# Performance work log

Measured on AMD Instinct MI355X. Metric: run time of the kernel, lower is better.

The kernel has to match this reference:

```python
import jax, jax.numpy as jnp
import numpy as np

S, T, D, H = 16384, 16, 128, 3   # statements, AST nodes per statement, feat dim, heads
N = S * T
EPS = 1e-5


def setup_inputs() -> dict:
    key = jax.random.key(0)
    k = jax.random.split(key, 12)
    idx = np.arange(N)
    child = idx[idx % T != 0]                      # chain edges child->parent within each AST
    src = jnp.asarray(np.concatenate([child, idx]), dtype=jnp.int32)       # + self loops
    dst = jnp.asarray(np.concatenate([child - 1, idx]), dtype=jnp.int32)
    sD = 1.0 / np.sqrt(D)
    s3D = 1.0 / np.sqrt(3.0 * D)
    return dict(
        x=jax.random.normal(k[0], (N, D), jnp.float32),
        W0=jax.random.normal(k[1], (D, H * D), jnp.float32) * sD,
        a_src0=jax.random.normal(k[2], (H, D), jnp.float32) * sD,
        a_dst0=jax.random.normal(k[3], (H, D), jnp.float32) * sD,
        b0=jnp.zeros((H * D,), jnp.float32),
        g0=jnp.ones((H * D,), jnp.float32),
        be0=jnp.zeros((H * D,), jnp.float32),
        W1=jax.random.normal(k[4], (H * D, D), jnp.float32) * s3D,
        a_src1=jax.random.normal(k[5], (1, D), jnp.float32) * sD,
        a_dst1=jax.random.normal(k[6], (1, D), jnp.float32) * sD,
        b1=jnp.zeros((D,), jnp.float32),
        g1=jnp.ones((D,), jnp.float32),
        be1=jnp.zeros((D,), jnp.float32),
        p=jax.random.normal(k[7], (D,), jnp.float32),
        mW1=jax.random.normal(k[8], (D, 32), jnp.float32) * sD,
        mb1=jnp.zeros((32,), jnp.float32),
        mW2=jax.random.normal(k[9], (32, D), jnp.float32) / np.sqrt(32.0),
        mb2=jnp.zeros((D,), jnp.float32),
        src=src,
        dst=dst,
    )


def _gat(x, W, a_s, a_d, b, src, dst, heads, out_c):
    # PyG GATConv (concat heads, leaky_relu 0.2, self-loops already in edge list)
    h = (x @ W).reshape(-1, heads, out_c)                 # [N,H,C]
    al_s = jnp.einsum('nhc,hc->nh', h, a_s)
    al_d = jnp.einsum('nhc,hc->nh', h, a_d)
    e = jax.nn.leaky_relu(al_s[src] + al_d[dst], 0.2)     # [E,H]
    m = jax.ops.segment_max(e, dst, num_segments=N)       # segment softmax over incoming edges
    ex = jnp.exp(e - m[dst])
    den = jax.ops.segment_sum(ex, dst, num_segments=N)
    alpha = ex / den[dst]
    out = jax.ops.segment_sum(alpha[:, :, None] * h[src], dst, num_segments=N)
    return out.reshape(-1, heads * out_c) + b


def _bn(x, g, b):
    mu = x.mean(0)
    var = x.var(0)
    return (x - mu) * jax.lax.rsqrt(var + EPS) * g + b


def reference(x, W0, a_src0, a_dst0, b0, g0, be0, W1, a_src1, a_dst1, b1, g1, be1, p, mW1, mb1, mW2, mb2, src, dst):
    h = _bn(jax.nn.relu(_gat(x, W0, a_src0, a_dst0, b0, src, dst, H, D)), g0, be0)
    h = _bn(jax.nn.relu(_gat(h, W1, a_src1, a_dst1, b1, src, dst, 1, D)), g1, be1)
    # TopKPooling (default ratio=0.5) per statement AST of T nodes
    s = (h @ p) / (jnp.linalg.norm(p) + 1e-16)            # [N]
    s = s.reshape(S, T)
    k = T // 2
    vals, idxk = jax.lax.top_k(s, k)                      # [S,k]
    hr = h.reshape(S, T, D)
    sel = jnp.take_along_axis(hr, idxk[:, :, None], axis=1) * jnp.tanh(vals)[:, :, None]
    pooled = jax.nn.relu(sel).mean(axis=1)                # [S,D] readout of kept nodes
    out = jax.nn.relu(pooled @ mW1 + mb1) @ mW2 + mb2     # MLP 128->32->128
    return out
```

## Files before the change

### kernel.cpp

```cpp
#include <hip/hip_runtime.h>
#include <math.h>

#define N_NODES 262144
#define SSTMT   16384
#define TT      16
#define DD      128
#define HH      3
#define HD      384
#define EPSV    1e-5f

__device__ __forceinline__ int swzc(int row, int c) { return c ^ (((row >> 3) & 3) << 2); }

template<int NTHR>
__device__ __forceinline__ void stageSwz(float (*dst)[DD], const float* __restrict__ src)
{
    const int tid = threadIdx.x;
    #pragma unroll
    for (int j = 0; j < 2048 / NTHR; ++j) {
        int gi = j * NTHR + tid;
        int row = gi >> 5;
        int c4 = (gi & 31) * 4;
        *reinterpret_cast<float4*>(&dst[row][swzc(row, c4)]) =
            *reinterpret_cast<const float4*>(&src[(size_t)row * DD + c4]);
    }
}

template<int BSTR, int KLEN>
__device__ __forceinline__ void gemm8x8(const float (*A)[DD], const float* __restrict__ Bbase,
                                        int kbeg, int rr, int pad, float acc[8][8])
{
    const float* bp = Bbase + (size_t)kbeg * BSTR;
    const float* ar = &A[rr * 8][0];
    #pragma unroll 2
    for (int k = 0; k < KLEN; k += 4) {
        float4 b00 = *reinterpret_cast<const float4*>(bp);
        float4 b01 = *reinterpret_cast<const float4*>(bp + 4);
        float4 b10 = *reinterpret_cast<const float4*>(bp + BSTR);
        float4 b11 = *reinterpret_cast<const float4*>(bp + BSTR + 4);
        float4 b20 = *reinterpret_cast<const float4*>(bp + 2 * BSTR);
        float4 b21 = *reinterpret_cast<const float4*>(bp + 2 * BSTR + 4);
        float4 b30 = *reinterpret_cast<const float4*>(bp + 3 * BSTR);
        float4 b31 = *reinterpret_cast<const float4*>(bp + 3 * BSTR + 4);
        bp += 4 * (size_t)BSTR;
        const int pc = (kbeg + k) ^ pad;
        #pragma unroll
        for (int i = 0; i < 8; ++i) {
            float4 a = *reinterpret_cast<const float4*>(ar + i * DD + pc);
            acc[i][0] += a.x*b00.x; acc[i][1] += a.x*b00.y; acc[i][2] += a.x*b00.z; acc[i][3] += a.x*b00.w;
            acc[i][4] += a.x*b01.x; acc[i][5] += a.x*b01.y; acc[i][6] += a.x*b01.z; acc[i][7] += a.x*b01.w;
            acc[i][0] += a.y*b10.x; acc[i][1] += a.y*b10.y; acc[i][2] += a.y*b10.z; acc[i][3] += a.y*b10.w;
            acc[i][4] += a.y*b11.x; acc[i][5] += a.y*b11.y; acc[i][6] += a.y*b11.z; acc[i][7] += a.y*b11.w;
            acc[i][0] += a.z*b20.x; acc[i][1] += a.z*b20.y; acc[i][2] += a.z*b20.z; acc[i][3] += a.z*b20.w;
            acc[i][4] += a.z*b21.x; acc[i][5] += a.z*b21.y; acc[i][6] += a.z*b21.z; acc[i][7] += a.z*b21.w;
            acc[i][0] += a.w*b30.x; acc[i][1] += a.w*b30.y; acc[i][2] += a.w*b30.z; acc[i][3] += a.w*b30.w;
            acc[i][4] += a.w*b31.x; acc[i][5] += a.w*b31.y; acc[i][6] += a.w*b31.z; acc[i][7] += a.w*b31.w;
        }
    }
}

__device__ __forceinline__ void attnAgg(float acc[8][8],
                                        const float* __restrict__ avsP,
                                        const float* __restrict__ avdP,
                                        const float* __restrict__ bP, int rr)
{
    float4 s0 = *reinterpret_cast<const float4*>(avsP);
    float4 s1 = *reinterpret_cast<const float4*>(avsP + 4);
    float4 d0 = *reinterpret_cast<const float4*>(avdP);
    float4 d1 = *reinterpret_cast<const float4*>(avdP + 4);
    float als[8], ald[8];
    #pragma unroll
    for (int i = 0; i < 8; ++i) {
        als[i] = acc[i][0]*s0.x + acc[i][1]*s0.y + acc[i][2]*s0.z + acc[i][3]*s0.w
               + acc[i][4]*s1.x + acc[i][5]*s1.y + acc[i][6]*s1.z + acc[i][7]*s1.w;
        ald[i] = acc[i][0]*d0.x + acc[i][1]*d0.y + acc[i][2]*d0.z + acc[i][3]*d0.w
               + acc[i][4]*d1.x + acc[i][5]*d1.y + acc[i][6]*d1.z + acc[i][7]*d1.w;
    }
    #pragma unroll
    for (int m = 1; m <= 8; m <<= 1) {
        #pragma unroll
        for (int i = 0; i < 8; ++i) {
            als[i] += __shfl_xor(als[i], m);
            ald[i] += __shfl_xor(ald[i], m);
        }
    }
    float alsN = __shfl_down(als[0], 16);
    float accN[8];
    #pragma unroll
    for (int j = 0; j < 8; ++j) accN[j] = __shfl_down(acc[0][j], 16);

    float4 bb0 = *reinterpret_cast<const float4*>(bP);
    float4 bb1 = *reinterpret_cast<const float4*>(bP + 4);
    float bbv[8] = {bb0.x, bb0.y, bb0.z, bb0.w, bb1.x, bb1.y, bb1.z, bb1.w};
    const bool tail7 = (rr & 1);
    #pragma unroll
    for (int i = 0; i < 8; ++i) {
        float es = als[i] + ald[i];
        es = es > 0.f ? es : 0.2f * es;
        float aS = 1.f, aN = 0.f;
        if (!(tail7 && i == 7)) {
            float en = ((i < 7) ? als[i + 1] : alsN) + ald[i];
            en = en > 0.f ? en : 0.2f * en;
            float mx = fmaxf(es, en);
            float e1 = expf(es - mx), e2 = expf(en - mx);
            float den = e1 + e2;
            aS = e1 / den; aN = e2 / den;
        }
        #pragma unroll
        for (int j = 0; j < 8; ++j) {
            float nb = (i < 7) ? acc[i + 1][j] : accN[j];
            acc[i][j] = fmaxf(aS * acc[i][j] + aN * nb + bbv[j], 0.f);
        }
    }
}

__global__ __launch_bounds__(128, 2)
void gat0_stats(const float* __restrict__ x, const float* __restrict__ W0,
                const float* __restrict__ as0, const float* __restrict__ ad0,
                const float* __restrict__ b0, float* __restrict__ pA0)
{
    __shared__ float xs[64][DD];
    __shared__ float bns[8][DD];

    const int tid = threadIdx.x;
    const int bid = blockIdx.x;
    const int rr = tid >> 4;
    const int cg = tid & 15;
    const int pad = (rr & 3) << 2;
    const size_t rb = (size_t)bid * 64;

    stageSwz<128>(xs, x + rb * DD);
    __syncthreads();

    float psum[HH][8], qsum[HH][8];
    #pragma unroll
    for (int h = 0; h < HH; ++h)
        #pragma unroll
        for (int j = 0; j < 8; ++j) { psum[h][j] = 0.f; qsum[h][j] = 0.f; }

    for (int h = 0; h < HH; ++h) {
        float acc[8][8];
        #pragma unroll
        for (int i = 0; i < 8; ++i)
            #pragma unroll
            for (int j = 0; j < 8; ++j) acc[i][j] = 0.f;

        gemm8x8<HD, 128>(xs, W0 + h * DD + cg * 8, 0, rr, pad, acc);
        attnAgg(acc, as0 + h * DD + cg * 8, ad0 + h * DD + cg * 8, b0 + h * DD + cg * 8, rr);

        #pragma unroll
        for (int i = 0; i < 8; ++i)
            #pragma unroll
            for (int j = 0; j < 8; ++j) {
                float o = acc[i][j];
                psum[h][j] += o; qsum[h][j] += o * o;
            }
    }

    for (int h = 0; h < HH; ++h) {
        __syncthreads();
        *reinterpret_cast<float4*>(&bns[rr][cg * 8]) =
            make_float4(psum[h][0], psum[h][1], psum[h][2], psum[h][3]);
        *reinterpret_cast<float4*>(&bns[rr][cg * 8 + 4]) =
            make_float4(psum[h][4], psum[h][5], psum[h][6], psum[h][7]);
        __syncthreads();
        float sv = 0.f;
        #pragma unroll
        for (int w = 0; w < 8; ++w) sv += bns[w][tid];
        __syncthreads();
        *reinterpret_cast<float4*>(&bns[rr][cg * 8]) =
            make_float4(qsum[h][0], qsum[h][1], qsum[h][2], qsum[h][3]);
        *reinterpret_cast<float4*>(&bns[rr][cg * 8 + 4]) =
            make_float4(qsum[h][4], qsum[h][5], qsum[h][6], qsum[h][7]);
        __syncthreads();
        float qv = 0.f;
        #pragma unroll
        for (int w = 0; w < 8; ++w) qv += bns[w][tid];
        size_t idx = ((size_t)bid * HD + h * DD + tid) * 2;
        pA0[idx] = sv; pA0[idx + 1] = qv;
    }
}

__global__ __launch_bounds__(256, 2)
void gat1_recomp(const float* __restrict__ x, const float* __restrict__ W0,
                 const float* __restrict__ as0, const float* __restrict__ ad0,
                 const float* __restrict__ b0, const float* __restrict__ sc0,
                 const float* __restrict__ sh0, const float* __restrict__ W1,
                 const float* __restrict__ as1, const float* __restrict__ ad1,
                 const float* __restrict__ b1,
                 float* __restrict__ r1, float* __restrict__ pA1)
{
    __shared__ float xs[64][DD];
    __shared__ float hs[64][DD];
    __shared__ float bps[8][DD], bqs[8][DD];

    const int tid = threadIdx.x;
    const int bid = blockIdx.x;
    const int kh = tid >> 7;
    const int rr = (tid >> 4) & 7;
    const int cg = tid & 15;
    const int pad = (rr & 3) << 2;
    const size_t rb = (size_t)bid * 64;

    stageSwz<256>(xs, x + rb * DD);
    __syncthreads();

    float acc2[8][8];
    #pragma unroll
    for (int i = 0; i < 8; ++i)
        #pragma unroll
        for (int j = 0; j < 8; ++j) acc2[i][j] = 0.f;

    for (int h = 0; h < HH; ++h) {
        float acc[8][8];
        #pragma unroll
        for (int i = 0; i < 8; ++i)
            #pragma unroll
            for (int j = 0; j < 8; ++j) acc[i][j] = 0.f;

        gemm8x8<HD, 64>(xs, W0 + h * DD + cg * 8, kh * 64, rr, pad, acc);

        __syncthreads();
        if (kh == 1) {
            #pragma unroll
            for (int i = 0; i < 8; ++i) {
                int pc = (cg * 8) ^ pad;
                *reinterpret_cast<float4*>(&hs[rr * 8 + i][pc]) =
                    make_float4(acc[i][0], acc[i][1], acc[i][2], acc[i][3]);
                *reinterpret_cast<float4*>(&hs[rr * 8 + i][pc ^ 4]) =
                    make_float4(acc[i][4], acc[i][5], acc[i][6], acc[i][7]);
            }
        }
        __syncthreads();
        if (kh == 0) {
            #pragma unroll
            for (int i = 0; i < 8; ++i) {
                int pc = (cg * 8) ^ pad;
                float4 p0 = *reinterpret_cast<const float4*>(&hs[rr * 8 + i][pc]);
                float4 p1 = *reinterpret_cast<const float4*>(&hs[rr * 8 + i][pc ^ 4]);
                acc[i][0] += p0.x; acc[i][1] += p0.y; acc[i][2] += p0.z; acc[i][3] += p0.w;
                acc[i][4] += p1.x; acc[i][5] += p1.y; acc[i][6] += p1.z; acc[i][7] += p1.w;
            }
            attnAgg(acc, as0 + h * DD + cg * 8, ad0 + h * DD + cg * 8, b0 + h * DD + cg * 8, rr);
            float4 sc0a = *reinterpret_cast<const float4*>(&sc0[h * DD + cg * 8]);
            float4 sc0b = *reinterpret_cast<const float4*>(&sc0[h * DD + cg * 8 + 4]);
            float4 sh0a = *reinterpret_cast<const float4*>(&sh0[h * DD + cg * 8]);
            float4 sh0b = *reinterpret_cast<const float4*>(&sh0[h * DD + cg * 8 + 4]);
            float scv[8] = {sc0a.x, sc0a.y, sc0a.z, sc0a.w, sc0b.x, sc0b.y, sc0b.z, sc0b.w};
            float shv[8] = {sh0a.x, sh0a.y, sh0a.z, sh0a.w, sh0b.x, sh0b.y, sh0b.z, sh0b.w};
            #pragma unroll
            for (int i = 0; i < 8; ++i) {
                int pc = (cg * 8) ^ pad;
                float v0 = acc[i][0] * scv[0] + shv[0];
                float v1 = acc[i][1] * scv[1] + shv[1];
                float v2 = acc[i][2] * scv[2] + shv[2];
                float v3 = acc[i][3] * scv[3] + shv[3];
                float v4 = acc[i][4] * scv[4] + shv[4];
                float v5 = acc[i][5] * scv[5] + shv[5];
                float v6 = acc[i][6] * scv[6] + shv[6];
                float v7 = acc[i][7] * scv[7] + shv[7];
                *reinterpret_cast<float4*>(&hs[rr * 8 + i][pc]) = make_float4(v0, v1, v2, v3);
                *reinterpret_cast<float4*>(&hs[rr * 8 + i][pc ^ 4]) = make_float4(v4, v5, v6, v7);
            }
        }
        __syncthreads();

        gemm8x8<DD, 64>(hs, W1 + (size_t)(h * DD) * DD + cg * 8, kh * 64, rr, pad, acc2);
    }

    __syncthreads();
    if (kh == 1) {
        #pragma unroll
        for (int i = 0; i < 8; ++i) {
            int pc = (cg * 8) ^ pad;
            *reinterpret_cast<float4*>(&xs[rr * 8 + i][pc]) =
                make_float4(acc2[i][0], acc2[i][1], acc2[i][2], acc2[i][3]);
            *reinterpret_cast<float4*>(&xs[rr * 8 + i][pc ^ 4]) =
                make_float4(acc2[i][4], acc2[i][5], acc2[i][6], acc2[i][7]);
        }
    }
    __syncthreads();
    if (kh == 0) {
        #pragma unroll
        for (int i = 0; i < 8; ++i) {
            int pc = (cg * 8) ^ pad;
            float4 p0 = *reinterpret_cast<const float4*>(&xs[rr * 8 + i][pc]);
            float4 p1 = *reinterpret_cast<const float4*>(&xs[rr * 8 + i][pc ^ 4]);
            acc2[i][0] += p0.x; acc2[i][1] += p0.y; acc2[i][2] += p0.z; acc2[i][3] += p0.w;
            acc2[i][4] += p1.x; acc2[i][5] += p1.y; acc2[i][6] += p1.z; acc2[i][7] += p1.w;
        }
        attnAgg(acc2, as1 + cg * 8, ad1 + cg * 8, b1 + cg * 8, rr);

        float ps[8], pq[8];
        #pragma unroll
        for (int j = 0; j < 8; ++j) { ps[j] = 0.f; pq[j] = 0.f; }
        #pragma unroll
        for (int i = 0; i < 8; ++i) {
            *reinterpret_cast<float4*>(&r1[(rb + rr * 8 + i) * DD + cg * 8]) =
                make_float4(acc2[i][0], acc2[i][1], acc2[i][2], acc2[i][3]);
            *reinterpret_cast<float4*>(&r1[(rb + rr * 8 + i) * DD + cg * 8 + 4]) =
                make_float4(acc2[i][4], acc2[i][5], acc2[i][6], acc2[i][7]);
            #pragma unroll
            for (int j = 0; j < 8; ++j) { ps[j] += acc2[i][j]; pq[j] += acc2[i][j] * acc2[i][j]; }
        }
        *reinterpret_cast<float4*>(&bps[rr][cg * 8])     = make_float4(ps[0], ps[1], ps[2], ps[3]);
        *reinterpret_cast<float4*>(&bps[rr][cg * 8 + 4]) = make_float4(ps[4], ps[5], ps[6], ps[7]);
        *reinterpret_cast<float4*>(&bqs[rr][cg * 8])     = make_float4(pq[0], pq[1], pq[2], pq[3]);
        *reinterpret_cast<float4*>(&bqs[rr][cg * 8 + 4]) = make_float4(pq[4], pq[5], pq[6], pq[7]);
    }
    __syncthreads();
    if (tid < 128) {
        float s = 0.f, q = 0.f;
        #pragma unroll
        for (int w = 0; w < 8; ++w) { s += bps[w][tid]; q += bqs[w][tid]; }
        size_t idx = ((size_t)bid * DD + tid) * 2;
        pA1[idx] = s; pA1[idx + 1] = q;
    }
}

__global__ __launch_bounds__(256)
void bn_reduce(const float* __restrict__ pA, int nblk, int ncol, float invN,
               const float* __restrict__ g, const float* __restrict__ be,
               float* __restrict__ sc, float* __restrict__ sh)
{
    __shared__ float rs[256], rq[256];
    int col = blockIdx.x, tid = threadIdx.x;
    float s = 0.f, q = 0.f;
    for (int i = tid; i < nblk; i += 256) {
        size_t idx = ((size_t)i * ncol + col) * 2;
        s += pA[idx]; q += pA[idx + 1];
    }
    rs[tid] = s; rq[tid] = q;
    __syncthreads();
    for (int o = 128; o > 0; o >>= 1) {
        if (tid < o) { rs[tid] += rs[tid + o]; rq[tid] += rq[tid + o]; }
        __syncthreads();
    }
    if (tid == 0) {
        float mu  = rs[0] * invN;
        float var = fmaxf(rq[0] * invN - mu * mu, 0.f);
        float inv = 1.0f / sqrtf(var + EPSV);
        float scv = g[col] * inv;
        sc[col] = scv;
        sh[col] = be[col] - mu * scv;
    }
}

__global__ __launch_bounds__(128)
void compute_pn(const float* __restrict__ p, float* __restrict__ pn)
{
    __shared__ float rs[128];
    int t = threadIdx.x;
    float v = p[t];
    rs[t] = v * v;
    __syncthreads();
    for (int o = 64; o > 0; o >>= 1) {
        if (t < o) rs[t] += rs[t + o];
        __syncthreads();
    }
    float nrm = sqrtf(rs[0]) + 1e-16f;
    pn[t] = v / nrm;
}

__global__ __launch_bounds__(128)
void pool_mlp(const float* __restrict__ r1, const float* __restrict__ sc1,
              const float* __restrict__ sh1, const float* __restrict__ pn,
              const float* __restrict__ mW1, const float* __restrict__ mb1,
              const float* __restrict__ mW2, const float* __restrict__ mb2,
              float* __restrict__ out)
{
    __shared__ float hf[16][136];
    __shared__ float sv[16];
    __shared__ float tv[16];
    __shared__ float pooled[128];
    __shared__ float y1[32];
    int tid = threadIdx.x;
    int sid = blockIdx.x;
    float scv = sc1[tid], shv = sh1[tid];
    const float* base = r1 + (size_t)sid * TT * DD;
    #pragma unroll
    for (int i = 0; i < 16; ++i)
        hf[i][tid] = base[i * DD + tid] * scv + shv;
    __syncthreads();

    {
        int r = tid >> 3, q = tid & 7;
        float s = 0.f;
        #pragma unroll
        for (int cc = 0; cc < 16; ++cc) {
            int c = q + cc * 8;
            s += hf[r][c] * pn[c];
        }
        s += __shfl_down(s, 4, 8);
        s += __shfl_down(s, 2, 8);
        s += __shfl_down(s, 1, 8);
        if (q == 0) sv[r] = s;
    }
    __syncthreads();

    if (tid < 16) {
        float si = sv[tid];
        int rank = 0;
        #pragma unroll
        for (int u = 0; u < 16; ++u) {
            float su = sv[u];
            rank += (su > si || (su == si && u < tid)) ? 1 : 0;
        }
        tv[tid] = (rank < 8) ? tanhf(si) : 0.f;
    }
    __syncthreads();

    {
        float a = 0.f;
        #pragma unroll
        for (int rr2 = 0; rr2 < 16; ++rr2)
            a += fmaxf(hf[rr2][tid] * tv[rr2], 0.f);
        pooled[tid] = a * 0.125f;
    }
    __syncthreads();

    {
        int j = tid >> 2, q = tid & 3;
        float a = 0.f;
        #pragma unroll
        for (int cc = 0; cc < 32; ++cc) {
            int c = q + cc * 4;
            a += pooled[c] * mW1[(size_t)c * 32 + j];
        }
        a += __shfl_down(a, 2, 4);
        a += __shfl_down(a, 1, 4);
        if (q == 0) y1[j] = fmaxf(a + mb1[j], 0.f);
    }
    __syncthreads();

    {
        float o = mb2[tid];
        #pragma unroll
        for (int j = 0; j < 32; ++j) o += y1[j] * mW2[j * 128 + tid];
        out[(size_t)sid * 128 + tid] = o;
    }
}

extern "C" void kernel_launch(void* const* d_in, const int* in_sizes, int n_in,
                              void* d_out, int out_size, void* d_ws, size_t ws_size,
                              hipStream_t stream)
{
    (void)in_sizes; (void)n_in; (void)out_size; (void)ws_size;
    const float* x   = (const float*)d_in[0];
    const float* W0  = (const float*)d_in[1];
    const float* as0 = (const float*)d_in[2];
    const float* ad0 = (const float*)d_in[3];
    const float* b0  = (const float*)d_in[4];
    const float* g0  = (const float*)d_in[5];
    const float* be0 = (const float*)d_in[6];
    const float* W1  = (const float*)d_in[7];
    const float* as1 = (const float*)d_in[8];
    const float* ad1 = (const float*)d_in[9];
    const float* b1  = (const float*)d_in[10];
    const float* g1  = (const float*)d_in[11];
    const float* be1 = (const float*)d_in[12];
    const float* p   = (const float*)d_in[13];
    const float* mW1 = (const float*)d_in[14];
    const float* mb1 = (const float*)d_in[15];
    const float* mW2 = (const float*)d_in[16];
    const float* mb2 = (const float*)d_in[17];
    float* out = (float*)d_out;

    const size_t R1B  = (size_t)N_NODES * DD * 4;
    const size_t PA0B = 4096ull * HD * 2 * 4;
    const size_t PA1B = 4096ull * DD * 2 * 4;

    char* ws = (char*)d_ws;
    float* r1  = (float*)ws;
    float* pA0 = (float*)(ws + R1B);
    float* pA1 = (float*)(ws + R1B + PA0B);
    float* vec = (float*)(ws + R1B + PA0B + PA1B);
    float* sc0 = vec;
    float* sh0 = vec + 512;
    float* sc1 = vec + 1024;
    float* sh1 = vec + 1536;
    float* pn  = vec + 2048;

    const float invN = 1.0f / (float)N_NODES;

    gat0_stats<<<N_NODES / 64, 128, 0, stream>>>(x, W0, as0, ad0, b0, pA0);
    bn_reduce<<<HD, 256, 0, stream>>>(pA0, N_NODES / 64, HD, invN, g0, be0, sc0, sh0);
    compute_pn<<<1, 128, 0, stream>>>(p, pn);
    gat1_recomp<<<N_NODES / 64, 256, 0, stream>>>(x, W0, as0, ad0, b0, sc0, sh0,
                                                  W1, as1, ad1, b1, r1, pA1);
    bn_reduce<<<DD, 256, 0, stream>>>(pA1, N_NODES / 64, DD, invN, g1, be1, sc1, sh1);
    pool_mlp<<<SSTMT, 128, 0, stream>>>(r1, sc1, sh1, pn, mW1, mb1, mW2, mb2, out);
}
```

Baseline: 1.117 ms.

## Split GEMM work by rows instead of K-halves in GAT kernels

Both GAT kernels switch from 8x8 per-thread tiles to 4x8 tiles over 256 threads. gat1_recomp no longer splits K across two thread halves, which removes the shared-memory partial-sum exchanges and extra barriers between them. gat0_stats doubles its threads per block and reduces per-head stats immediately, so it no longer keeps all three heads' sums in registers. The A-tile swizzle is adjusted to match the new row mapping. In exchange, the B (weight) loads are reused across fewer rows per thread, so more global/L1 weight traffic is issued per FMA.

```diff
diff --git a/kernel.cpp b/kernel.cpp
--- a/kernel.cpp
+++ b/kernel.cpp
@@ -9,15 +9,14 @@
 #define HD      384
 #define EPSV    1e-5f
 
-__device__ __forceinline__ int swzc(int row, int c) { return c ^ (((row >> 3) & 3) << 2); }
-
-template<int NTHR>
+__device__ __forceinline__ int swzc(int row, int c) { return c ^ (((row >> 2) & 3) << 2); }
+
 __device__ __forceinline__ void stageSwz(float (*dst)[DD], const float* __restrict__ src)
 {
     const int tid = threadIdx.x;
     #pragma unroll
-    for (int j = 0; j < 2048 / NTHR; ++j) {
-        int gi = j * NTHR + tid;
+    for (int j = 0; j < 8; ++j) {
+        int gi = j * 256 + tid;
         int row = gi >> 5;
         int c4 = (gi & 31) * 4;
         *reinterpret_cast<float4*>(&dst[row][swzc(row, c4)]) =
@@ -25,51 +24,65 @@
     }
 }
 
-template<int BSTR, int KLEN>
-__device__ __forceinline__ void gemm8x8(const float (*A)[DD], const float* __restrict__ Bbase,
-                                        int kbeg, int rr, int pad, float acc[8][8])
-{
-    const float* bp = Bbase + (size_t)kbeg * BSTR;
-    const float* ar = &A[rr * 8][0];
+#define FMA8(s, bl, bh, i)                                    \
+    acc[i][0] += s * bl.x; acc[i][1] += s * bl.y;             \
+    acc[i][2] += s * bl.z; acc[i][3] += s * bl.w;             \
+    acc[i][4] += s * bh.x; acc[i][5] += s * bh.y;             \
+    acc[i][6] += s * bh.z; acc[i][7] += s * bh.w;
+
+template<int BSTR>
+__device__ __forceinline__ void gemm4x8(const float (*A)[DD], const float* __restrict__ Bg,
+                                        int rowBase, int pad, float acc[4][8])
+{
+    const float* ar = &A[rowBase][0];
+    const float* bp = Bg;
     #pragma unroll 2
-    for (int k = 0; k < KLEN; k += 4) {
-        float4 b00 = *reinterpret_cast<const float4*>(bp);
-        float4 b01 = *reinterpret_cast<const float4*>(bp + 4);
-        float4 b10 = *reinterpret_cast<const float4*>(bp + BSTR);
-        float4 b11 = *reinterpret_cast<const float4*>(bp + BSTR + 4);
-        float4 b20 = *reinterpret_cast<const float4*>(bp + 2 * BSTR);
-        float4 b21 = *reinterpret_cast<const float4*>(bp + 2 * BSTR + 4);
-        float4 b30 = *reinterpret_cast<const float4*>(bp + 3 * BSTR);
-        float4 b31 = *reinterpret_cast<const float4*>(bp + 3 * BSTR + 4);
-        bp += 4 * (size_t)BSTR;
-        const int pc = (kbeg + k) ^ pad;
-        #pragma unroll
-        for (int i = 0; i < 8; ++i) {
-            float4 a = *reinterpret_cast<const float4*>(ar + i * DD + pc);
-            acc[i][0] += a.x*b00.x; acc[i][1] += a.x*b00.y; acc[i][2] += a.x*b00.z; acc[i][3] += a.x*b00.w;
-            acc[i][4] += a.x*b01.x; acc[i][5] += a.x*b01.y; acc[i][6] += a.x*b01.z; acc[i][7] += a.x*b01.w;
-            acc[i][0] += a.y*b10.x; acc[i][1] += a.y*b10.y; acc[i][2] += a.y*b10.z; acc[i][3] += a.y*b10.w;
-            acc[i][4] += a.y*b11.x; acc[i][5] += a.y*b11.y; acc[i][6] += a.y*b11.z; acc[i][7] += a.y*b11.w;
-            acc[i][0] += a.z*b20.x; acc[i][1] += a.z*b20.y; acc[i][2] += a.z*b20.z; acc[i][3] += a.z*b20.w;
-            acc[i][4] += a.z*b21.x; acc[i][5] += a.z*b21.y; acc[i][6] += a.z*b21.z; acc[i][7] += a.z*b21.w;
-            acc[i][0] += a.w*b30.x; acc[i][1] += a.w*b30.y; acc[i][2] += a.w*b30.z; acc[i][3] += a.w*b30.w;
-            acc[i][4] += a.w*b31.x; acc[i][5] += a.w*b31.y; acc[i][6] += a.w*b31.z; acc[i][7] += a.w*b31.w;
-        }
-    }
-}
-
-__device__ __forceinline__ void attnAgg(float acc[8][8],
-                                        const float* __restrict__ avsP,
-                                        const float* __restrict__ avdP,
-                                        const float* __restrict__ bP, int rr)
+    for (int k = 0; k < 128; k += 4) {
+        int pc = k ^ pad;
+        float4 a0 = *reinterpret_cast<const float4*>(ar + 0 * DD + pc);
+        float4 a1 = *reinterpret_cast<const float4*>(ar + 1 * DD + pc);
+        float4 a2 = *reinterpret_cast<const float4*>(ar + 2 * DD + pc);
+        float4 a3 = *reinterpret_cast<const float4*>(ar + 3 * DD + pc);
+        {
+            float4 bl = *reinterpret_cast<const float4*>(bp);
+            float4 bh = *reinterpret_cast<const float4*>(bp + 4);
+            FMA8(a0.x, bl, bh, 0) FMA8(a1.x, bl, bh, 1)
+            FMA8(a2.x, bl, bh, 2) FMA8(a3.x, bl, bh, 3)
+        }
+        {
+            float4 bl = *reinterpret_cast<const float4*>(bp + BSTR);
+            float4 bh = *reinterpret_cast<const float4*>(bp + BSTR + 4);
+            FMA8(a0.y, bl, bh, 0) FMA8(a1.y, bl, bh, 1)
+            FMA8(a2.y, bl, bh, 2) FMA8(a3.y, bl, bh, 3)
+        }
+        {
+            float4 bl = *reinterpret_cast<const float4*>(bp + 2 * BSTR);
+            float4 bh = *reinterpret_cast<const float4*>(bp + 2 * BSTR + 4);
+            FMA8(a0.z, bl, bh, 0) FMA8(a1.z, bl, bh, 1)
+            FMA8(a2.z, bl, bh, 2) FMA8(a3.z, bl, bh, 3)
+        }
+        {
+            float4 bl = *reinterpret_cast<const float4*>(bp + 3 * BSTR);
+            float4 bh = *reinterpret_cast<const float4*>(bp + 3 * BSTR + 4);
+            FMA8(a0.w, bl, bh, 0) FMA8(a1.w, bl, bh, 1)
+            FMA8(a2.w, bl, bh, 2) FMA8(a3.w, bl, bh, 3)
+        }
+        bp += 4 * BSTR;
+    }
+}
+
+__device__ __forceinline__ void attnAgg4(float acc[4][8],
+                                         const float* __restrict__ avsP,
+                                         const float* __restrict__ avdP,
+                                         const float* __restrict__ bP, int rl)
 {
     float4 s0 = *reinterpret_cast<const float4*>(avsP);
     float4 s1 = *reinterpret_cast<const float4*>(avsP + 4);
     float4 d0 = *reinterpret_cast<const float4*>(avdP);
     float4 d1 = *reinterpret_cast<const float4*>(avdP + 4);
-    float als[8], ald[8];
-    #pragma unroll
-    for (int i = 0; i < 8; ++i) {
+    float als[4], ald[4];
+    #pragma unroll
+    for (int i = 0; i < 4; ++i) {
         als[i] = acc[i][0]*s0.x + acc[i][1]*s0.y + acc[i][2]*s0.z + acc[i][3]*s0.w
                + acc[i][4]*s1.x + acc[i][5]*s1.y + acc[i][6]*s1.z + acc[i][7]*s1.w;
         ald[i] = acc[i][0]*d0.x + acc[i][1]*d0.y + acc[i][2]*d0.z + acc[i][3]*d0.w
@@ -78,7 +91,7 @@
     #pragma unroll
     for (int m = 1; m <= 8; m <<= 1) {
         #pragma unroll
-        for (int i = 0; i < 8; ++i) {
+        for (int i = 0; i < 4; ++i) {
             als[i] += __shfl_xor(als[i], m);
             ald[i] += __shfl_xor(ald[i], m);
         }
@@ -91,14 +104,14 @@
     float4 bb0 = *reinterpret_cast<const float4*>(bP);
     float4 bb1 = *reinterpret_cast<const float4*>(bP + 4);
     float bbv[8] = {bb0.x, bb0.y, bb0.z, bb0.w, bb1.x, bb1.y, bb1.z, bb1.w};
-    const bool tail7 = (rr & 1);
-    #pragma unroll
-    for (int i = 0; i < 8; ++i) {
+    const bool tail = (rl == 3);
+    #pragma unroll
+    for (int i = 0; i < 4; ++i) {
         float es = als[i] + ald[i];
         es = es > 0.f ? es : 0.2f * es;
         float aS = 1.f, aN = 0.f;
-        if (!(tail7 && i == 7)) {
-            float en = ((i < 7) ? als[i + 1] : alsN) + ald[i];
+        if (!(tail && i == 3)) {
+            float en = ((i < 3) ? als[i + 1] : alsN) + ald[i];
             en = en > 0.f ? en : 0.2f * en;
             float mx = fmaxf(es, en);
             float e1 = expf(es - mx), e2 = expf(en - mx);
@@ -107,76 +120,73 @@
         }
         #pragma unroll
         for (int j = 0; j < 8; ++j) {
-            float nb = (i < 7) ? acc[i + 1][j] : accN[j];
+            float nb = (i < 3) ? acc[i + 1][j] : accN[j];
             acc[i][j] = fmaxf(aS * acc[i][j] + aN * nb + bbv[j], 0.f);
         }
     }
 }
 
-__global__ __launch_bounds__(128, 2)
+__global__ __launch_bounds__(256, 2)
 void gat0_stats(const float* __restrict__ x, const float* __restrict__ W0,
                 const float* __restrict__ as0, const float* __restrict__ ad0,
                 const float* __restrict__ b0, float* __restrict__ pA0)
 {
     __shared__ float xs[64][DD];
-    __shared__ float bns[8][DD];
+    __shared__ float bns[16][DD];
 
     const int tid = threadIdx.x;
     const int bid = blockIdx.x;
     const int rr = tid >> 4;
-    const int cg = tid & 15;
-    const int pad = (rr & 3) << 2;
+    const int cgg = tid & 15;
+    const int rl = rr & 3;
+    const int pad = rl << 2;
+    const int rowBase = rr * 4;
     const size_t rb = (size_t)bid * 64;
 
-    stageSwz<128>(xs, x + rb * DD);
-    __syncthreads();
-
-    float psum[HH][8], qsum[HH][8];
-    #pragma unroll
-    for (int h = 0; h < HH; ++h)
-        #pragma unroll
-        for (int j = 0; j < 8; ++j) { psum[h][j] = 0.f; qsum[h][j] = 0.f; }
+    stageSwz(xs, x + rb * DD);
+    __syncthreads();
 
     for (int h = 0; h < HH; ++h) {
-        float acc[8][8];
-        #pragma unroll
-        for (int i = 0; i < 8; ++i)
+        float acc[4][8];
+        #pragma unroll
+        for (int i = 0; i < 4; ++i)
             #pragma unroll
             for (int j = 0; j < 8; ++j) acc[i][j] = 0.f;
 
-        gemm8x8<HD, 128>(xs, W0 + h * DD + cg * 8, 0, rr, pad, acc);
-        attnAgg(acc, as0 + h * DD + cg * 8, ad0 + h * DD + cg * 8, b0 + h * DD + cg * 8, rr);
-
-        #pragma unroll
-        for (int i = 0; i < 8; ++i)
+        gemm4x8<HD>(xs, W0 + h * DD + cgg * 8, rowBase, pad, acc);
+        attnAgg4(acc, as0 + h * DD + cgg * 8, ad0 + h * DD + cgg * 8, b0 + h * DD + cgg * 8, rl);
+
+        float ps[8], pq[8];
+        #pragma unroll
+        for (int j = 0; j < 8; ++j) { ps[j] = 0.f; pq[j] = 0.f; }
+        #pragma unroll
+        for (int i = 0; i < 4; ++i)
             #pragma unroll
             for (int j = 0; j < 8; ++j) {
                 float o = acc[i][j];
-                psum[h][j] += o; qsum[h][j] += o * o;
+                ps[j] += o; pq[j] += o * o;
             }
-    }
-
-    for (int h = 0; h < HH; ++h) {
-        __syncthreads();
-        *reinterpret_cast<float4*>(&bns[rr][cg * 8]) =
-            make_float4(psum[h][0], psum[h][1], psum[h][2], psum[h][3]);
-        *reinterpret_cast<float4*>(&bns[rr][cg * 8 + 4]) =
-            make_float4(psum[h][4], psum[h][5], psum[h][6], psum[h][7]);
+
+        __syncthreads();
+        *reinterpret_cast<float4*>(&bns[rr][cgg * 8])     = make_float4(ps[0], ps[1], ps[2], ps[3]);
+        *reinterpret_cast<float4*>(&bns[rr][cgg * 8 + 4]) = make_float4(ps[4], ps[5], ps[6], ps[7]);
         __syncthreads();
         float sv = 0.f;
-        #pragma unroll
-        for (int w = 0; w < 8; ++w) sv += bns[w][tid];
-        __syncthreads();
-        *reinterpret_cast<float4*>(&bns[rr][cg * 8]) =
-            make_float4(qsum[h][0], qsum[h][1], qsum[h][2], qsum[h][3]);
-        *reinterpret_cast<float4*>(&bns[rr][cg * 8 + 4]) =
-            make_float4(qsum[h][4], qsum[h][5], qsum[h][6], qsum[h][7]);
-        __syncthreads();
-        float qv = 0.f;
-        #pragma unroll
-        for (int w = 0; w < 8; ++w) qv += bns[w][tid];
-        size_t idx = ((size_t)bid * HD + h * DD + tid) * 2;
-        pA0[idx] = sv; pA0[idx + 1] = qv;
+        if (tid < 128) {
+            #pragma unroll
+            for (int w = 0; w < 16; ++w) sv += bns[w][tid];
+        }
+        __syncthreads();
+        *reinterpret_cast<float4*>(&bns[rr][cgg * 8])     = make_float4(pq[0], pq[1], pq[2], pq[3]);
+        *reinterpret_cast<float4*>(&bns[rr][cgg * 8 + 4]) = make_float4(pq[4], pq[5], pq[6], pq[7]);
+        __syncthreads();
+        if (tid < 128) {
+            float qv = 0.f;
+            #pragma unroll
+            for (int w = 0; w < 16; ++w) qv += bns[w][tid];
+            size_t idx = ((size_t)bid * HD + h * DD + tid) * 2;
+            pA0[idx] = sv; pA0[idx + 1] = qv;
+        }
     }
 }
 
@@ -191,129 +201,101 @@
 {
     __shared__ float xs[64][DD];
     __shared__ float hs[64][DD];
-    __shared__ float bps[8][DD], bqs[8][DD];
 
     const int tid = threadIdx.x;
     const int bid = blockIdx.x;
-    const int kh = tid >> 7;
-    const int rr = (tid >> 4) & 7;
-    const int cg = tid & 15;
-    const int pad = (rr & 3) << 2;
+    const int rr = tid >> 4;
+    const int cgg = tid & 15;
+    const int rl = rr & 3;
+    const int pad = rl << 2;
+    const int rowBase = rr * 4;
     const size_t rb = (size_t)bid * 64;
 
-    stageSwz<256>(xs, x + rb * DD);
-    __syncthreads();
-
-    float acc2[8][8];
-    #pragma unroll
-    for (int i = 0; i < 8; ++i)
+    stageSwz(xs, x + rb * DD);
+    __syncthreads();
+
+    float acc2[4][8];
+    #pragma unroll
+    for (int i = 0; i < 4; ++i)
         #pragma unroll
         for (int j = 0; j < 8; ++j) acc2[i][j] = 0.f;
 
     for (int h = 0; h < HH; ++h) {
-        float acc[8][8];
-        #pragma unroll
-        for (int i = 0; i < 8; ++i)
+        float acc[4][8];
+        #pragma unroll
+        for (int i = 0; i < 4; ++i)
             #pragma unroll
             for (int j = 0; j < 8; ++j) acc[i][j] = 0.f;
 
-        gemm8x8<HD, 64>(xs, W0 + h * DD + cg * 8, kh * 64, rr, pad, acc);
-
-        __syncthreads();
-        if (kh == 1) {
-            #pragma unroll
-            for (int i = 0; i < 8; ++i) {
-                int pc = (cg * 8) ^ pad;
-                *reinterpret_cast<float4*>(&hs[rr * 8 + i][pc]) =
+        gemm4x8<HD>(xs, W0 + h * DD + cgg * 8, rowBase, pad, acc);
+        attnAgg4(acc, as0 + h * DD + cgg * 8, ad0 + h * DD + cgg * 8, b0 + h * DD + cgg * 8, rl);
+
+        {
+            float4 sa = *reinterpret_cast<const float4*>(&sc0[h * DD + cgg * 8]);
+            float4 sb = *reinterpret_cast<const float4*>(&sc0[h * DD + cgg * 8 + 4]);
+            float4 ha = *reinterpret_cast<const float4*>(&sh0[h * DD + cgg * 8]);
+            float4 hb = *reinterpret_cast<const float4*>(&sh0[h * DD + cgg * 8 + 4]);
+            float scv[8] = {sa.x, sa.y, sa.z, sa.w, sb.x, sb.y, sb.z, sb.w};
+            float shv[8] = {ha.x, ha.y, ha.z, ha.w, hb.x, hb.y, hb.z, hb.w};
+            #pragma unroll
+            for (int i = 0; i < 4; ++i)
+                #pragma unroll
+                for (int j = 0; j < 8; ++j)
+                    acc[i][j] = acc[i][j] * scv[j] + shv[j];
+        }
+
+        __syncthreads();
+        {
+            int pcA = (cgg * 8) ^ pad;
+            int pcB = pcA ^ 4;
+            #pragma unroll
+            for (int i = 0; i < 4; ++i) {
+                *reinterpret_cast<float4*>(&hs[rowBase + i][pcA]) =
                     make_float4(acc[i][0], acc[i][1], acc[i][2], acc[i][3]);
-                *reinterpret_cast<float4*>(&hs[rr * 8 + i][pc ^ 4]) =
+                *reinterpret_cast<float4*>(&hs[rowBase + i][pcB]) =
                     make_float4(acc[i][4], acc[i][5], acc[i][6], acc[i][7]);
             }
         }
         __syncthreads();
-        if (kh == 0) {
-            #pragma unroll
-            for (int i = 0; i < 8; ++i) {
-                int pc = (cg * 8) ^ pad;
-                float4 p0 = *reinterpret_cast<const float4*>(&hs[rr * 8 + i][pc]);
-                float4 p1 = *reinterpret_cast<const float4*>(&hs[rr * 8 + i][pc ^ 4]);
-                acc[i][0] += p0.x; acc[i][1] += p0.y; acc[i][2] += p0.z; acc[i][3] += p0.w;
-                acc[i][4] += p1.x; acc[i][5] += p1.y; acc[i][6] += p1.z; acc[i][7] += p1.w;
-            }
-            attnAgg(acc, as0 + h * DD + cg * 8, ad0 + h * DD + cg * 8, b0 + h * DD + cg * 8, rr);
-            float4 sc0a = *reinterpret_cast<const float4*>(&sc0[h * DD + cg * 8]);
-            float4 sc0b = *reinterpret_cast<const float4*>(&sc0[h * DD + cg * 8 + 4]);
-            float4 sh0a = *reinterpret_cast<const float4*>(&sh0[h * DD + cg * 8]);
-            float4 sh0b = *reinterpret_cast<const float4*>(&sh0[h * DD + cg * 8 + 4]);
-            float scv[8] = {sc0a.x, sc0a.y, sc0a.z, sc0a.w, sc0b.x, sc0b.y, sc0b.z, sc0b.w};
-            float shv[8] = {sh0a.x, sh0a.y, sh0a.z, sh0a.w, sh0b.x, sh0b.y, sh0b.z, sh0b.w};
-            #pragma unroll
-            for (int i = 0; i < 8; ++i) {
-                int pc = (cg * 8) ^ pad;
-                float v0 = acc[i][0] * scv[0] + shv[0];
-                float v1 = acc[i][1] * scv[1] + shv[1];
-                float v2 = acc[i][2] * scv[2] + shv[2];
-                float v3 = acc[i][3] * scv[3] + shv[3];
-                float v4 = acc[i][4] * scv[4] + shv[4];
-                float v5 = acc[i][5] * scv[5] + shv[5];
-                float v6 = acc[i][6] * scv[6] + shv[6];
-                float v7 = acc[i][7] * scv[7] + shv[7];
-                *reinterpret_cast<float4*>(&hs[rr * 8 + i][pc]) = make_float4(v0, v1, v2, v3);
-                *reinterpret_cast<float4*>(&hs[rr * 8 + i][pc ^ 4]) = make_float4(v4, v5, v6, v7);
-            }
-        }
-        __syncthreads();
-
-        gemm8x8<DD, 64>(hs, W1 + (size_t)(h * DD) * DD + cg * 8, kh * 64, rr, pad, acc2);
-    }
-
-    __syncthreads();
-    if (kh == 1) {
-        #pragma unroll
-        for (int i = 0; i < 8; ++i) {
-            int pc = (cg * 8) ^ pad;
-            *reinterpret_cast<float4*>(&xs[rr * 8 + i][pc]) =
-                make_float4(acc2[i][0], acc2[i][1], acc2[i][2], acc2[i][3]);
-            *reinterpret_cast<float4*>(&xs[rr * 8 + i][pc ^ 4]) =
-                make_float4(acc2[i][4], acc2[i][5], acc2[i][6], acc2[i][7]);
-        }
-    }
-    __syncthreads();
-    if (kh == 0) {
-        #pragma unroll
-        for (int i = 0; i < 8; ++i) {
-            int pc = (cg * 8) ^ pad;
-            float4 p0 = *reinterpret_cast<const float4*>(&xs[rr * 8 + i][pc]);
-            float4 p1 = *reinterpret_cast<const float4*>(&xs[rr * 8 + i][pc ^ 4]);
-            acc2[i][0] += p0.x; acc2[i][1] += p0.y; acc2[i][2] += p0.z; acc2[i][3] += p0.w;
-            acc2[i][4] += p1.x; acc2[i][5] += p1.y; acc2[i][6] += p1.z; acc2[i][7] += p1.w;
-        }
-        attnAgg(acc2, as1 + cg * 8, ad1 + cg * 8, b1 + cg * 8, rr);
-
-        float ps[8], pq[8];
-        #pragma unroll
-        for (int j = 0; j < 8; ++j) { ps[j] = 0.f; pq[j] = 0.f; }
-        #pragma unroll
-        for (int i = 0; i < 8; ++i) {
-            *reinterpret_cast<float4*>(&r1[(rb + rr * 8 + i) * DD + cg * 8]) =
-                make_float4(acc2[i][0], acc2[i][1], acc2[i][2], acc2[i][3]);
-            *reinterpret_cast<float4*>(&r1[(rb + rr * 8 + i) * DD + cg * 8 + 4]) =
-                make_float4(acc2[i][4], acc2[i][5], acc2[i][6], acc2[i][7]);
-            #pragma unroll
-            for (int j = 0; j < 8; ++j) { ps[j] += acc2[i][j]; pq[j] += acc2[i][j] * acc2[i][j]; }
-        }
-        *reinterpret_cast<float4*>(&bps[rr][cg * 8])     = make_float4(ps[0], ps[1], ps[2], ps[3]);
-        *reinterpret_cast<float4*>(&bps[rr][cg * 8 + 4]) = make_float4(ps[4], ps[5], ps[6], ps[7]);
-        *reinterpret_cast<float4*>(&bqs[rr][cg * 8])     = make_float4(pq[0], pq[1], pq[2], pq[3]);
-        *reinterpret_cast<float4*>(&bqs[rr][cg * 8 + 4]) = make_float4(pq[4], pq[5], pq[6], pq[7]);
-    }
-    __syncthreads();
+
+        gemm4x8<DD>(hs, W1 + (size_t)(h * DD) * DD + cgg * 8, rowBase, pad, acc2);
+    }
+
+    attnAgg4(acc2, as1 + cgg * 8, ad1 + cgg * 8, b1 + cgg * 8, rl);
+
+    float ps[8], pq[8];
+    #pragma unroll
+    for (int j = 0; j < 8; ++j) { ps[j] = 0.f; pq[j] = 0.f; }
+    #pragma unroll
+    for (int i = 0; i < 4; ++i) {
+        *reinterpret_cast<float4*>(&r1[(rb + rowBase + i) * DD + cgg * 8]) =
+            make_float4(acc2[i][0], acc2[i][1], acc2[i][2], acc2[i][3]);
+        *reinterpret_cast<float4*>(&r1[(rb + rowBase + i) * DD + cgg * 8 + 4]) =
+            make_float4(acc2[i][4], acc2[i][5], acc2[i][6], acc2[i][7]);
+        #pragma unroll
+        for (int j = 0; j < 8; ++j) { ps[j] += acc2[i][j]; pq[j] += acc2[i][j] * acc2[i][j]; }
+    }
+
+    float (*bns)[DD] = xs;
+    __syncthreads();
+    *reinterpret_cast<float4*>(&bns[rr][cgg * 8])     = make_float4(ps[0], ps[1], ps[2], ps[3]);
+    *reinterpret_cast<float4*>(&bns[rr][cgg * 8 + 4]) = make_float4(ps[4], ps[5], ps[6], ps[7]);
+    __syncthreads();
+    float sv = 0.f;
     if (tid < 128) {
-        float s = 0.f, q = 0.f;
-        #pragma unroll
-        for (int w = 0; w < 8; ++w) { s += bps[w][tid]; q += bqs[w][tid]; }
+        #pragma unroll
+        for (int w = 0; w < 16; ++w) sv += bns[w][tid];
+    }
+    __syncthreads();
+    *reinterpret_cast<float4*>(&bns[rr][cgg * 8])     = make_float4(pq[0], pq[1], pq[2], pq[3]);
+    *reinterpret_cast<float4*>(&bns[rr][cgg * 8 + 4]) = make_float4(pq[4], pq[5], pq[6], pq[7]);
+    __syncthreads();
+    if (tid < 128) {
+        float qv = 0.f;
+        #pragma unroll
+        for (int w = 0; w < 16; ++w) qv += bns[w][tid];
         size_t idx = ((size_t)bid * DD + tid) * 2;
-        pA1[idx] = s; pA1[idx + 1] = q;
+        pA1[idx] = sv; pA1[idx + 1] = qv;
     }
 }
 
@@ -482,7 +464,7 @@
 
     const float invN = 1.0f / (float)N_NODES;
 
-    gat0_stats<<<N_NODES / 64, 128, 0, stream>>>(x, W0, as0, ad0, b0, pA0);
+    gat0_stats<<<N_NODES / 64, 256, 0, stream>>>(x, W0, as0, ad0, b0, pA0);
     bn_reduce<<<HD, 256, 0, stream>>>(pA0, N_NODES / 64, HD, invN, g0, be0, sc0, sh0);
     compute_pn<<<1, 128, 0, stream>>>(p, pn);
     gat1_recomp<<<N_NODES / 64, 256, 0, stream>>>(x, W0, as0, ad0, b0, sc0, sh0,
```

After: 1.232 ms. 10.3% more time.
